# Kernel optimization log

Hardware: AMD Instinct MI355X
Metric: run time of the kernel (lower is better)

Reference implementation:

```python
import jax, jax.numpy as jnp
import numpy as np

B, F, E, H = 4096, 26, 64, 1000000
D = F * E  # 1664

def setup_inputs() -> dict:
    key = jax.random.key(0)
    ks = jax.random.split(key, 12)
    s = 0.02  # init scale
    return {
        "ids": jax.random.randint(ks[0], (B, F), 0, H),
        "emb": jax.random.normal(ks[1], (H, E), jnp.float32) * s,
        "cross_w": jax.random.normal(ks[2], (3, D), jnp.float32) * s,
        "cross_b": jnp.zeros((3, D), jnp.float32),
        "w1": jax.random.normal(ks[3], (D, 1024), jnp.float32) * s,
        "b1": jnp.zeros((1024,), jnp.float32),
        "w2": jax.random.normal(ks[4], (1024, 512), jnp.float32) * s,
        "b2": jnp.zeros((512,), jnp.float32),
        "w3": jax.random.normal(ks[5], (512, 256), jnp.float32) * s,
        "b3": jnp.zeros((256,), jnp.float32),
        "out_w": jax.random.normal(ks[6], (D + 256, 1), jnp.float32) * s,
        "out_b": jnp.zeros((), jnp.float32),
    }

def reference(ids, emb, cross_w, cross_b, w1, b1, w2, b2, w3, b3, out_w, out_b):
    # Embedding lookup + field-wise concat -> x0: [B, D]
    x0 = emb[ids].reshape(ids.shape[0], -1)
    # Cross net. Original materializes [B,D,D] outer product x0 * x^T then
    # giving the same math with O(B*D) memory.
    x = x0
    for i in range(cross_w.shape[0]):
        s = x @ cross_w[i]                 # [B] per-example scalar
        x = x0 * s[:, None] + cross_b[i] + x
    # Deep tower on x0
    h = jax.nn.relu(x0 @ w1 + b1)
    h = jax.nn.relu(h @ w2 + b2)
    h = jax.nn.relu(h @ w3 + b3)
    # Output head
    logit = jnp.concatenate([x, h], axis=1) @ out_w + out_b  # [B, 1]
    return jax.nn.sigmoid(logit)
```

## Files before the change

kernel.cpp:

```cpp
#include <hip/hip_runtime.h>
#include <hip/hip_bf16.h>

#define B_  4096
#define F_  26
#define E_  64
#define D_  1664
#define N1_ 1024
#define N2_ 512
#define N3_ 256

typedef __attribute__((ext_vector_type(8))) __bf16 bf16x8;
typedef __attribute__((ext_vector_type(4))) float  f32x4;

__device__ __forceinline__ unsigned short f2b(float x) {
    __hip_bfloat16 h = __float2bfloat16(x);
    return __builtin_bit_cast(unsigned short, h);
}
__device__ __forceinline__ float b2f(unsigned short u) {
    return __uint_as_float(((unsigned)u) << 16);
}

__device__ __forceinline__ void async_load16(const void* g, void* l) {
    __builtin_amdgcn_global_load_lds(
        (const __attribute__((address_space(1))) void*)g,
        (__attribute__((address_space(3))) void*)l,
        16, 0, 0);
}

__device__ __forceinline__ f32x4 mfma16(bf16x8 a, bf16x8 b, f32x4 c) {
    return __builtin_amdgcn_mfma_f32_16x16x32_bf16(a, b, c, 0, 0, 0);
}

__global__ __launch_bounds__(256) void gather_cross_transpose_kernel(
        const int* __restrict__ ids, const float* __restrict__ emb,
        const float* __restrict__ cw, const float* __restrict__ cb,
        const float* __restrict__ out_w,
        unsigned short* __restrict__ x0out, float* __restrict__ partial,
        const float* __restrict__ w1, const float* __restrict__ w2,
        const float* __restrict__ w3,
        unsigned short* __restrict__ o1, unsigned short* __restrict__ o2,
        unsigned short* __restrict__ o3)
{
    __shared__ int   sid[F_];
    __shared__ float red[2][4];
    __shared__ float tile[32][33];

    if (blockIdx.x >= B_) {
        const int bid = blockIdx.x - B_;
        const float* in; unsigned short* out; int K, N, lg, t0;
        if (bid < 1664)      { in = w1; out = o1; K = D_;  N = N1_; lg = 5; t0 = 0;    }
        else if (bid < 2176) { in = w2; out = o2; K = N1_; N = N2_; lg = 4; t0 = 1664; }
        else                 { in = w3; out = o3; K = N2_; N = N3_; lg = 3; t0 = 2176; }
        const int tl = bid - t0;
        const int n0 = (tl & ((1 << lg) - 1)) * 32;
        const int k0 = (tl >> lg) * 32;
        const int tc = threadIdx.x & 31, tr = threadIdx.x >> 5;
        #pragma unroll
        for (int p = 0; p < 4; p++)
            tile[tr + p * 8][tc] = in[(size_t)(k0 + tr + p * 8) * N + n0 + tc];
        __syncthreads();
        #pragma unroll
        for (int p = 0; p < 4; p++) {
            const int n = tr + p * 8;
            out[(size_t)(n0 + n) * K + k0 + tc] = f2b(tile[tc][n]);
        }
        return;
    }

    const int b = blockIdx.x;
    const int t = threadIdx.x;
    const int lane = t & 63, w = t >> 6;
    constexpr int C4 = D_ / 4;

    if (t < F_) sid[t] = ids[b * F_ + t];
    __syncthreads();

    const float4* emb4 = (const float4*)emb;
    const float4* cw4  = (const float4*)cw;
    const float4* cb4  = (const float4*)cb;
    const float4* ow4  = (const float4*)out_w;

    float4 x0v[2], xv[2];
    #pragma unroll
    for (int j = 0; j < 2; j++) {
        const int c = t + j * 256;
        float4 v = make_float4(0.f, 0.f, 0.f, 0.f);
        if (c < C4) {
            const int f = c >> 4;
            v = emb4[(size_t)sid[f] * 16 + (c & 15)];
            ushort4 o;
            o.x = f2b(v.x); o.y = f2b(v.y); o.z = f2b(v.z); o.w = f2b(v.w);
            ((ushort4*)x0out)[(size_t)b * C4 + c] = o;
        }
        x0v[j] = v; xv[j] = v;
    }
    for (int i = 0; i < 3; i++) {
        float s = 0.f;
        #pragma unroll
        for (int j = 0; j < 2; j++) {
            const int c = t + j * 256;
            if (c < C4) {
                const float4 wv = cw4[i * C4 + c];
                s += xv[j].x * wv.x + xv[j].y * wv.y + xv[j].z * wv.z + xv[j].w * wv.w;
            }
        }
        #pragma unroll
        for (int off = 32; off > 0; off >>= 1) s += __shfl_down(s, off, 64);
        if (lane == 0) red[i & 1][w] = s;
        __syncthreads();
        const float st = red[i & 1][0] + red[i & 1][1] + red[i & 1][2] + red[i & 1][3];
        #pragma unroll
        for (int j = 0; j < 2; j++) {
            const int c = t + j * 256;
            if (c < C4) {
                const float4 bv = cb4[i * C4 + c];
                xv[j].x = x0v[j].x * st + bv.x + xv[j].x;
                xv[j].y = x0v[j].y * st + bv.y + xv[j].y;
                xv[j].z = x0v[j].z * st + bv.z + xv[j].z;
                xv[j].w = x0v[j].w * st + bv.w + xv[j].w;
            }
        }
    }
    float s = 0.f;
    #pragma unroll
    for (int j = 0; j < 2; j++) {
        const int c = t + j * 256;
        if (c < C4) {
            const float4 wv = ow4[c];
            s += xv[j].x * wv.x + xv[j].y * wv.y + xv[j].z * wv.z + xv[j].w * wv.w;
        }
    }
    #pragma unroll
    for (int off = 32; off > 0; off >>= 1) s += __shfl_down(s, off, 64);
    if (lane == 0) red[1][w] = s;
    __syncthreads();
    if (t == 0) partial[b] = red[1][0] + red[1][1] + red[1][2] + red[1][3];
}

template<int BM, int BN, int BKC>
__global__ __launch_bounds__(256, 4) void gemm_bias_relu(
        const unsigned short* __restrict__ A,
        const unsigned short* __restrict__ Bt,
        const float* __restrict__ bias,
        unsigned short* __restrict__ C,
        int M, int N, int K)
{
    constexpr int KU = BKC / 32;
    constexpr int WM = BM / 2, WN = BN / 2;
    constexpr int TI = WM / 16, TJ = WN / 16;
    constexpr int nA = BM / 16, nB = BN / 16, nAB = nA + nB;
    constexpr int TOTC = KU * nAB;
    static_assert(TOTC % 4 == 0, "chunk loop assumes 4-wave coverage");

    __shared__ unsigned short sA[KU * BM * 32];
    __shared__ unsigned short sB[KU * BN * 32];

    const int t    = threadIdx.x;
    const int lane = t & 63;
    const int w    = t >> 6;

    const int i    = blockIdx.y * gridDim.x + blockIdx.x;
    const int xcd  = i & 7;
    const int s    = i >> 3;
    const int ypg  = gridDim.y >> 3;
    const int ty   = xcd * ypg + s / gridDim.x;
    const int tx   = s - (s / gridDim.x) * gridDim.x;
    const int m0   = ty * BM;
    const int n0   = tx * BN;
    const int wm   = (w >> 1) * WM;
    const int wn   = (w & 1) * WN;

    const int srow = lane >> 2;
    const int scol = (lane & 3) * 8;

    f32x4 acc[TI][TJ] = {};

    for (int k0 = 0; k0 < K; k0 += BKC) {
        #pragma unroll
        for (int c0 = 0; c0 < TOTC; c0 += 4) {
            const int c = c0 + w;
            const int u = c / nAB;
            const int r = c - u * nAB;
            if (r < nA) {
                const unsigned short* g =
                    A + (size_t)(m0 + r * 16 + srow) * K + k0 + u * 32 + scol;
                async_load16(g, &sA[u * BM * 32 + r * 512]);
            } else {
                const int rb = r - nA;
                const unsigned short* g =
                    Bt + (size_t)(n0 + rb * 16 + srow) * K + k0 + u * 32 + scol;
                async_load16(g, &sB[u * BN * 32 + rb * 512]);
            }
        }
        __syncthreads();

        #pragma unroll
        for (int u = 0; u < KU; u++) {
            bf16x8 af[TI], bf[TJ];
            #pragma unroll
            for (int ii = 0; ii < TI; ii++)
                af[ii] = *(const bf16x8*)
                    &sA[u * BM * 32 + (wm + ii * 16 + (lane & 15)) * 32 + (lane >> 4) * 8];
            #pragma unroll
            for (int j = 0; j < TJ; j++)
                bf[j] = *(const bf16x8*)
                    &sB[u * BN * 32 + (wn + j * 16 + (lane & 15)) * 32 + (lane >> 4) * 8];
            #pragma unroll
            for (int ii = 0; ii < TI; ii++)
                #pragma unroll
                for (int j = 0; j < TJ; j++)
                    acc[ii][j] = mfma16(af[ii], bf[j], acc[ii][j]);
        }
        __syncthreads();
    }

    #pragma unroll
    for (int ii = 0; ii < TI; ii++) {
        const int r0 = m0 + wm + ii * 16 + (lane >> 4) * 4;
        #pragma unroll
        for (int j = 0; j < TJ; j++) {
            const int col = n0 + wn + j * 16 + (lane & 15);
            const float bv = bias[col];
            #pragma unroll
            for (int r = 0; r < 4; r++) {
                float v = acc[ii][j][r] + bv;
                v = fmaxf(v, 0.f);
                C[(size_t)(r0 + r) * N + col] = f2b(v);
            }
        }
    }
}

__global__ __launch_bounds__(256) void head_kernel(
        const float* __restrict__ partial, const unsigned short* __restrict__ h3,
        const float* __restrict__ out_w, const float* __restrict__ out_b,
        float* __restrict__ out)
{
    const int gw   = (blockIdx.x * 256 + threadIdx.x) >> 6;
    const int lane = threadIdx.x & 63;
    if (gw >= B_) return;
    float s = 0.f;
    #pragma unroll
    for (int q = 0; q < 4; q++) {
        const int j = lane + q * 64;
        s += b2f(h3[(size_t)gw * N3_ + j]) * out_w[D_ + j];
    }
    #pragma unroll
    for (int off = 32; off > 0; off >>= 1) s += __shfl_down(s, off, 64);
    if (lane == 0) {
        const float logit = partial[gw] + s + out_b[0];
        out[gw] = 1.f / (1.f + expf(-logit));
    }
}

extern "C" void kernel_launch(void* const* d_in, const int* in_sizes, int n_in,
                              void* d_out, int out_size, void* d_ws, size_t ws_size,
                              hipStream_t stream)
{
    (void)in_sizes; (void)n_in; (void)out_size; (void)ws_size;
    const int*   ids     = (const int*)  d_in[0];
    const float* emb     = (const float*)d_in[1];
    const float* cross_w = (const float*)d_in[2];
    const float* cross_b = (const float*)d_in[3];
    const float* w1      = (const float*)d_in[4];
    const float* b1      = (const float*)d_in[5];
    const float* w2      = (const float*)d_in[6];
    const float* b2      = (const float*)d_in[7];
    const float* w3      = (const float*)d_in[8];
    const float* b3      = (const float*)d_in[9];
    const float* out_w   = (const float*)d_in[10];
    const float* out_b   = (const float*)d_in[11];
    float* out = (float*)d_out;

    char* p = (char*)d_ws;
    auto alloc = [&](size_t bytes) {
        char* r = p; p += (bytes + 255) & ~(size_t)255; return r;
    };
    unsigned short* x0b = (unsigned short*)alloc((size_t)B_ * D_ * 2);
    unsigned short* w1t = (unsigned short*)alloc((size_t)D_ * N1_ * 2);
    unsigned short* w2t = (unsigned short*)alloc((size_t)N1_ * N2_ * 2);
    unsigned short* w3t = (unsigned short*)alloc((size_t)N2_ * N3_ * 2);
    unsigned short* h1  = (unsigned short*)alloc((size_t)B_ * N1_ * 2);
    unsigned short* h2  = (unsigned short*)alloc((size_t)B_ * N2_ * 2);
    unsigned short* h3  = (unsigned short*)alloc((size_t)B_ * N3_ * 2);
    float* partial      = (float*)alloc((size_t)B_ * 4);

    for (int rep = 0; rep < 2; rep++) {
        gather_cross_transpose_kernel<<<B_ + 2304, 256, 0, stream>>>(
            ids, emb, cross_w, cross_b, out_w, x0b, partial,
            w1, w2, w3, w1t, w2t, w3t);

        gemm_bias_relu<64, 64, 128><<<dim3(N1_ / 64, B_ / 64), 256, 0, stream>>>(
            x0b, w1t, b1, h1, B_, N1_, D_);
        gemm_bias_relu<64, 32, 128><<<dim3(N2_ / 32, B_ / 64), 256, 0, stream>>>(
            h1, w2t, b2, h2, B_, N2_, N1_);
        gemm_bias_relu<32, 32, 128><<<dim3(N3_ / 32, B_ / 32), 256, 0, stream>>>(
            h2, w3t, b3, h3, B_, N3_, N2_);

        head_kernel<<<B_ / 4, 256, 0, stream>>>(partial, h3, out_w, out_b, out);
    }
}
```

Before: 446.3 us.

## Add double-buffered GEMM1 kernel and drop redundant second pipeline pass

```diff
diff --git a/kernel.cpp b/kernel.cpp
--- a/kernel.cpp
+++ b/kernel.cpp
@@ -135,6 +135,112 @@
     if (lane == 0) red[1][w] = s;
     __syncthreads();
     if (t == 0) partial[b] = red[1][0] + red[1][1] + red[1][2] + red[1][3];
+}
+
+__global__ __launch_bounds__(256, 2) void gemm1_pipe(
+        const unsigned short* __restrict__ A,
+        const unsigned short* __restrict__ Bt,
+        const float* __restrict__ bias,
+        unsigned short* __restrict__ C)
+{
+    constexpr int M = B_, N = N1_, K = D_;
+    constexpr int BM = 128, BN = 64, BKC = 64, KU = BKC / 32;
+    constexpr int nA = BM / 16, nB = BN / 16, nAB = nA + nB;
+    constexpr int TOTC = KU * nAB;
+    constexpr int T = K / BKC;
+    constexpr int LPW = TOTC / 4;
+    static_assert(LPW == 6 && (nA % 4) == 0, "chunk schedule");
+
+    __shared__ unsigned short sA[2][KU * BM * 32];
+    __shared__ unsigned short sB[2][KU * BN * 32];
+
+    const int t    = threadIdx.x;
+    const int lane = t & 63;
+    const int w    = t >> 6;
+
+    const int i    = blockIdx.y * gridDim.x + blockIdx.x;
+    const int xcd  = i & 7;
+    const int s    = i >> 3;
+    const int ypg  = gridDim.y >> 3;
+    const int ty   = xcd * ypg + s / gridDim.x;
+    const int tx   = s - (s / gridDim.x) * gridDim.x;
+    const int m0   = ty * BM;
+    const int n0   = tx * BN;
+    const int wm   = (w >> 1) * 64;
+    const int wn   = (w & 1) * 32;
+
+    const int srow = lane >> 2;
+    const int scol = ((lane & 3) ^ ((lane >> 3) & 3)) * 8;
+    const int rcol = (((lane >> 4) ^ ((lane >> 1) & 3))) * 8;
+
+    f32x4 acc[4][2] = {};
+
+    auto STAGE = [&](int kt, int bsel) {
+        const int k0 = kt * BKC;
+        #pragma unroll
+        for (int c0 = 0; c0 < TOTC; c0 += 4) {
+            const int c = c0 + w;
+            const int u = c / nAB;
+            const int r = c - u * nAB;
+            if (r < nA) {
+                const unsigned short* g =
+                    A + (size_t)(m0 + r * 16 + srow) * K + k0 + u * 32 + scol;
+                async_load16(g, &sA[bsel][u * BM * 32 + r * 512]);
+            } else {
+                const int rb = r - nA;
+                const unsigned short* g =
+                    Bt + (size_t)(n0 + rb * 16 + srow) * K + k0 + u * 32 + scol;
+                async_load16(g, &sB[bsel][u * BN * 32 + rb * 512]);
+            }
+        }
+    };
+
+    STAGE(0, 0);
+    for (int kt = 0; kt < T; kt++) {
+        const int cur = kt & 1;
+        if (kt + 1 < T) {
+            STAGE(kt + 1, cur ^ 1);
+            asm volatile("s_waitcnt vmcnt(6)" ::: "memory");
+        } else {
+            asm volatile("s_waitcnt vmcnt(0)" ::: "memory");
+        }
+        __builtin_amdgcn_s_barrier();
+        __builtin_amdgcn_sched_barrier(0);
+        #pragma unroll
+        for (int u = 0; u < KU; u++) {
+            bf16x8 af[4], bfr[2];
+            #pragma unroll
+            for (int ii = 0; ii < 4; ii++)
+                af[ii] = *(const bf16x8*)
+                    &sA[cur][u * BM * 32 + (wm + ii * 16 + (lane & 15)) * 32 + rcol];
+            #pragma unroll
+            for (int j = 0; j < 2; j++)
+                bfr[j] = *(const bf16x8*)
+                    &sB[cur][u * BN * 32 + (wn + j * 16 + (lane & 15)) * 32 + rcol];
+            #pragma unroll
+            for (int ii = 0; ii < 4; ii++)
+                #pragma unroll
+                for (int j = 0; j < 2; j++)
+                    acc[ii][j] = mfma16(af[ii], bfr[j], acc[ii][j]);
+        }
+        __builtin_amdgcn_s_barrier();
+    }
+
+    #pragma unroll
+    for (int ii = 0; ii < 4; ii++) {
+        const int r0 = m0 + wm + ii * 16 + (lane >> 4) * 4;
+        #pragma unroll
+        for (int j = 0; j < 2; j++) {
+            const int col = n0 + wn + j * 16 + (lane & 15);
+            const float bv = bias[col];
+            #pragma unroll
+            for (int r = 0; r < 4; r++) {
+                float v = acc[ii][j][r] + bv;
+                v = fmaxf(v, 0.f);
+                C[(size_t)(r0 + r) * N + col] = f2b(v);
+            }
+        }
+    }
 }
 
 template<int BM, int BN, int BKC>
@@ -285,18 +391,15 @@
     unsigned short* h3  = (unsigned short*)alloc((size_t)B_ * N3_ * 2);
     float* partial      = (float*)alloc((size_t)B_ * 4);
 
-    for (int rep = 0; rep < 2; rep++) {
-        gather_cross_transpose_kernel<<<B_ + 2304, 256, 0, stream>>>(
-            ids, emb, cross_w, cross_b, out_w, x0b, partial,
-            w1, w2, w3, w1t, w2t, w3t);
-
-        gemm_bias_relu<64, 64, 128><<<dim3(N1_ / 64, B_ / 64), 256, 0, stream>>>(
-            x0b, w1t, b1, h1, B_, N1_, D_);
-        gemm_bias_relu<64, 32, 128><<<dim3(N2_ / 32, B_ / 64), 256, 0, stream>>>(
-            h1, w2t, b2, h2, B_, N2_, N1_);
-        gemm_bias_relu<32, 32, 128><<<dim3(N3_ / 32, B_ / 32), 256, 0, stream>>>(
-            h2, w3t, b3, h3, B_, N3_, N2_);
-
-        head_kernel<<<B_ / 4, 256, 0, stream>>>(partial, h3, out_w, out_b, out);
-    }
-}
+    gather_cross_transpose_kernel<<<B_ + 2304, 256, 0, stream>>>(
+        ids, emb, cross_w, cross_b, out_w, x0b, partial,
+        w1, w2, w3, w1t, w2t, w3t);
+
+    gemm1_pipe<<<dim3(N1_ / 64, B_ / 128), 256, 0, stream>>>(x0b, w1t, b1, h1);
+    gemm_bias_relu<64, 32, 128><<<dim3(N2_ / 32, B_ / 64), 256, 0, stream>>>(
+        h1, w2t, b2, h2, B_, N2_, N1_);
+    gemm_bias_relu<32, 32, 128><<<dim3(N3_ / 32, B_ / 32), 256, 0, stream>>>(
+        h2, w3t, b3, h3, B_, N3_, N2_);
+
+    head_kernel<<<B_ / 4, 256, 0, stream>>>(partial, h3, out_w, out_b, out);
+}
```

Result: faster. 371.6 us (-16.7%).
